# Kernel optimization log

Measured on AMD Instinct MI355X. Metric: run time of the kernel, lower is better.

The kernel has to match this reference:

```python
import jax, jax.numpy as jnp
import numpy as np
from jax.ops import segment_sum, segment_max

E = 300000
H = 256
NC = 20000
EPS = 1e-6
RESIDUAL_UNIFORM = 0.2


def setup_inputs() -> dict:
    key = jax.random.key(0)
    k = jax.random.split(key, 6)
    edge_repr = jax.random.normal(k[0], (E, H), dtype=jnp.float32)
    edge_weight = jax.random.uniform(k[1], (E,), dtype=jnp.float32)
    case_idx = jax.random.randint(k[2], (E,), 0, NC)
    W1 = jax.random.normal(k[3], (4 * H, H), dtype=jnp.float32) * (1.0 / np.sqrt(4 * H))
    b1 = jnp.zeros((H,), dtype=jnp.float32)
    W2 = jax.random.normal(k[4], (H, 1), dtype=jnp.float32) * (1.0 / np.sqrt(H))
    b2 = jnp.zeros((1,), dtype=jnp.float32)
    return {"edge_repr": edge_repr, "edge_weight": edge_weight, "case_idx": case_idx,
            "num_case": NC, "W1": W1, "b1": b1, "W2": W2, "b2": b2}


def reference(edge_repr, edge_weight, case_idx, num_case, W1, b1, W2, b2):
    # --- leave-one-out context per edge ---
    weighted = edge_repr * edge_weight[:, None]                       # [E,H]
    case_deg = segment_sum(edge_weight, case_idx, num_segments=num_case)   # [NC]
    case_sum = segment_sum(weighted, case_idx, num_segments=num_case)      # [NC,H]
    base_case_repr = case_sum / jnp.maximum(case_deg, EPS)[:, None]        # [NC,H]

    edge_case_deg = case_deg[case_idx][:, None]                       # [E,1]
    w2d = edge_weight[:, None]
    remaining = edge_case_deg - w2d
    ctx_loocv = (case_sum[case_idx] - weighted) / jnp.maximum(remaining, 1e-8)
    fallback = (remaining <= EPS).astype(edge_repr.dtype)
    ctx = fallback * base_case_repr[case_idx] + (1.0 - fallback) * ctx_loocv  # [E,H]

    # --- attention MLP on [e, ctx, e*ctx, |e-ctx|] ---
    feat = jnp.concatenate([edge_repr, ctx, edge_repr * ctx,
                            jnp.abs(edge_repr - ctx)], axis=-1)       # [E,4H]
    h = jax.nn.relu(feat @ W1 + b1)                                   # [E,H] (dropout = identity in eval)
    logits = (h @ W2 + b2)[:, 0]                                      # [E]

    # --- grouped (per-case) stable softmax ---
    gmax = segment_max(logits, case_idx, num_segments=num_case)
    gmax = jnp.where(jnp.isneginf(gmax), jnp.zeros_like(gmax), gmax)
    exp_val = jnp.exp(logits - gmax[case_idx])
    gsum = segment_sum(exp_val, case_idx, num_segments=num_case)
    alpha = exp_val / (gsum[case_idx] + 1e-8)

    uniform_alpha = edge_weight / (case_deg[case_idx] + 1e-8)
    final_alpha = (1.0 - RESIDUAL_UNIFORM) * alpha + RESIDUAL_UNIFORM * uniform_alpha

    case_repr = segment_sum(final_alpha[:, None] * edge_repr, case_idx,
                            num_segments=num_case)                    # [NC,H]
    return case_repr
```

## Files before the change

kernel.cpp:

```cpp
#include <hip/hip_runtime.h>
#include <hip/hip_bf16.h>
#include <math.h>

#define H 256
#define EPSV 1e-6f

typedef __attribute__((ext_vector_type(8))) short bf16x8;
typedef __attribute__((ext_vector_type(4))) float f32x4;
typedef __attribute__((ext_vector_type(4))) unsigned int uint4v;

static __device__ __forceinline__ unsigned short f2bf(float x){
  union { float f; unsigned u; } v; v.f = x;
  unsigned r = v.u + 0x7FFF + ((v.u >> 16) & 1);
  return (unsigned short)(r >> 16);
}
static __device__ __forceinline__ unsigned pk2(unsigned short lo, unsigned short hi){
  return (unsigned)lo | ((unsigned)hi << 16);
}

__global__ void count_kernel(const int* __restrict__ cidx, int* __restrict__ counts, int E){
  int e = blockIdx.x * blockDim.x + threadIdx.x;
  if (e < E) atomicAdd(&counts[cidx[e]], 1);
}

__global__ __launch_bounds__(1024) void scan_offsets(const int* __restrict__ counts,
                                                     int* __restrict__ offsets, int n){
  __shared__ int a[1024];
  int tid = threadIdx.x;
  int per = (n + 1023) >> 10;
  int start = tid * per;
  int end = min(start + per, n);
  int s = 0;
  for (int i = start; i < end; ++i) s += counts[i];
  a[tid] = s;
  __syncthreads();
  for (int d = 1; d < 1024; d <<= 1){
    int v = 0;
    if (tid >= d) v = a[tid - d];
    __syncthreads();
    if (tid >= d) a[tid] += v;
    __syncthreads();
  }
  int run = a[tid] - s;
  for (int i = start; i < end; ++i){ offsets[i] = run; run += counts[i]; }
  if (tid == 1023) offsets[n] = a[1023];
}

__global__ void fill_kernel(const int* __restrict__ cidx, int* __restrict__ cursor,
                            const int* __restrict__ offs, int* __restrict__ elist, int E){
  int e = blockIdx.x * blockDim.x + threadIdx.x;
  if (e < E){
    int c = cidx[e];
    int pos = atomicAdd(&cursor[c], 1);
    elist[offs[c] + pos] = e;
  }
}

__global__ __launch_bounds__(64) void sort_lists(int* __restrict__ elist,
                                                 const int* __restrict__ offs, int nc){
  int c = blockIdx.x, lane = threadIdx.x;
  int s = offs[c], e = offs[c + 1];
  int n = e - s;
  if (n <= 1) return;
  __shared__ int vals[128];
  if (n <= 128){
    int v0 = (lane < n)      ? elist[s + lane]      : 0;
    int v1 = (64 + lane < n) ? elist[s + 64 + lane] : 0;
    vals[lane] = v0; vals[64 + lane] = v1;
    __syncthreads();
    int r0 = 0, r1 = 0;
    for (int j = 0; j < n; ++j){
      int vj = vals[j];
      r0 += (vj < v0); r1 += (vj < v1);
    }
    if (lane < n)      elist[s + r0] = v0;
    if (64 + lane < n) elist[s + r1] = v1;
  } else if (lane == 0){
    for (int i = s + 1; i < e; ++i){
      int v = elist[i];
      int j = i - 1;
      while (j >= s && elist[j] > v){ elist[j + 1] = elist[j]; --j; }
      elist[j + 1] = v;
    }
  }
}

__global__ void w1_convert(const float* __restrict__ W1, unsigned short* __restrict__ w1t2){
  int t = blockIdx.x * blockDim.x + threadIdx.x;
  int k = t >> 8, n = t & 255;
  w1t2[((size_t)(k >> 5) * 256 + n) * 32 + (k & 31)] = f2bf(W1[t]);
}

__global__ __launch_bounds__(64) void case_sums(const float* __restrict__ er,
                                                const float* __restrict__ ew,
                                                const int* __restrict__ elist,
                                                const int* __restrict__ offs,
                                                float* __restrict__ csum,
                                                float* __restrict__ cdeg){
  int c = blockIdx.x, lane = threadIdx.x;
  int s = offs[c], e = offs[c + 1];
  f32x4 acc = (f32x4){0.f,0.f,0.f,0.f};
  float dacc = 0.f;
  int i = s;
  for (; i + 1 < e; i += 2){
    int e1 = elist[i], e2 = elist[i + 1];
    float w1 = ew[e1], w2 = ew[e2];
    f32x4 v1 = *(const f32x4*)&er[(size_t)e1 * H + lane * 4];
    f32x4 v2 = *(const f32x4*)&er[(size_t)e2 * H + lane * 4];
    acc += v1 * w1;
    acc += v2 * w2;
    dacc += w1; dacc += w2;
  }
  if (i < e){
    int e1 = elist[i];
    float w1 = ew[e1];
    acc += (*(const f32x4*)&er[(size_t)e1 * H + lane * 4]) * w1;
    dacc += w1;
  }
  *(f32x4*)&csum[(size_t)c * H + lane * 4] = acc;
  if (lane == 0) cdeg[c] = dacc;
}

__global__ __launch_bounds__(256, 2) void fused_mlp(
    const float* __restrict__ er, const float* __restrict__ ew,
    const int* __restrict__ cidx, const float* __restrict__ cdeg,
    const float* __restrict__ csum, const unsigned short* __restrict__ w1t2,
    const float* __restrict__ b1, const float* __restrict__ w2,
    const float* __restrict__ b2, float* __restrict__ logits, int E)
{
  __shared__ unsigned short fl[4][64 * 64];
  __shared__ float lpart[4][64];
  int tid = threadIdx.x;
  long e0 = (long)blockIdx.x * 64;

  int wn = tid >> 6, lane = tid & 63;
  int l15 = lane & 15, lg = lane >> 4;

  int r = tid >> 2, q = tid & 3;
  long e = e0 + r;
  bool valid = (e < (long)E);
  int   cce = valid ? cidx[e] : 0;
  float w   = valid ? ew[e]   : 0.f;
  float deg = valid ? cdeg[cce] : 1.f;
  float rem = deg - w;
  bool  fb  = (rem <= EPSV);
  float inv  = fb ? (1.0f / fmaxf(deg, EPSV)) : (1.0f / fmaxf(rem, 1e-8f));
  float wsel = fb ? 0.f : w;
  const float* erow = er   + (size_t)e   * H + q * 16;
  const float* srow = csum + (size_t)cce * H + q * 16;
  unsigned rowb = (unsigned)r * 64u;
  unsigned swz  = ((unsigned)(r & 7)) << 3;

  f32x4 acc[4][4];
  #pragma unroll
  for (int mt = 0; mt < 4; ++mt)
    #pragma unroll
    for (int nt = 0; nt < 4; ++nt) acc[mt][nt] = (f32x4){0.f,0.f,0.f,0.f};

  unsigned bpcol = ((unsigned)(wn * 64 + l15)) * 32u + (unsigned)lg * 8u;

  f32x4 xr[4] = {(f32x4){0,0,0,0},(f32x4){0,0,0,0},(f32x4){0,0,0,0},(f32x4){0,0,0,0}};
  f32x4 sr[4] = {(f32x4){0,0,0,0},(f32x4){0,0,0,0},(f32x4){0,0,0,0},(f32x4){0,0,0,0}};

#define LOADQ(QT)                                                         \
  if (valid){                                                             \
    _Pragma("unroll")                                                     \
    for (int j = 0; j < 4; ++j){                                          \
      xr[j] = *(const f32x4*)(erow + (QT) * 64 + 4 * j);                  \
      sr[j] = *(const f32x4*)(srow + (QT) * 64 + 4 * j);                  \
    }                                                                     \
  }

#define CLUSTER(CL)                                                       \
  {                                                                       \
    const int kg_ = ((CL) & 3) * 8 + qt * 2 + ((CL) >> 2);                \
    bf16x8 bfr[4];                                                        \
    _Pragma("unroll")                                                     \
    for (int nt = 0; nt < 4; ++nt)                                        \
      bfr[nt] = *(const bf16x8*)(w1t2 + (size_t)kg_ * 8192 + nt * 512 + bpcol); \
    const int sg_ = (CL) & 3;                                             \
    unsigned eb_ = (unsigned)(((CL) >> 2) * 32 + lg * 8);                 \
    _Pragma("unroll")                                                     \
    for (int mt = 0; mt < 4; ++mt){                                       \
      unsigned row_ = (unsigned)(mt * 16 + l15);                          \
      unsigned off_ = row_ * 64u + (eb_ ^ ((row_ & 7u) << 3));            \
      bf16x8 af_ = *(const bf16x8*)&fl[sg_][off_];                        \
      _Pragma("unroll")                                                   \
      for (int nt = 0; nt < 4; ++nt)                                      \
        acc[mt][nt] = __builtin_amdgcn_mfma_f32_16x16x32_bf16(af_, bfr[nt], acc[mt][nt], 0, 0, 0); \
    }                                                                     \
  }

  LOADQ(0)

  #pragma unroll
  for (int qt = 0; qt < 4; ++qt){
    #pragma unroll
    for (int j2 = 0; j2 < 2; ++j2){
      unsigned xw[4], cw[4], pw[4], dw[4];
      #pragma unroll
      for (int d = 0; d < 4; ++d){
        float x0 = xr[2*j2 + (d>>1)][(d&1)*2+0], x1 = xr[2*j2 + (d>>1)][(d&1)*2+1];
        float s0 = sr[2*j2 + (d>>1)][(d&1)*2+0], s1 = sr[2*j2 + (d>>1)][(d&1)*2+1];
        float c0 = (s0 - wsel * x0) * inv;
        float c1 = (s1 - wsel * x1) * inv;
        xw[d] = pk2(f2bf(x0), f2bf(x1));
        cw[d] = pk2(f2bf(c0), f2bf(c1));
        pw[d] = pk2(f2bf(x0 * c0), f2bf(x1 * c1));
        dw[d] = pk2(f2bf(fabsf(x0 - c0)), f2bf(fabsf(x1 - c1)));
      }
      unsigned elem = (unsigned)(q * 16 + j2 * 8);
      unsigned off  = rowb + (elem ^ swz);
      *(uint4v*)&fl[0][off] = (uint4v){xw[0], xw[1], xw[2], xw[3]};
      *(uint4v*)&fl[1][off] = (uint4v){cw[0], cw[1], cw[2], cw[3]};
      *(uint4v*)&fl[2][off] = (uint4v){pw[0], pw[1], pw[2], pw[3]};
      *(uint4v*)&fl[3][off] = (uint4v){dw[0], dw[1], dw[2], dw[3]};
    }
    __syncthreads();
    if (qt == 0){ LOADQ(1) } else if (qt == 1){ LOADQ(2) } else if (qt == 2){ LOADQ(3) }

    CLUSTER(0) CLUSTER(1) CLUSTER(2) CLUSTER(3)
    CLUSTER(4) CLUSTER(5) CLUSTER(6) CLUSTER(7)
    __syncthreads();
  }
#undef LOADQ
#undef CLUSTER

  float p[4][4];
  #pragma unroll
  for (int mt = 0; mt < 4; ++mt)
    #pragma unroll
    for (int j = 0; j < 4; ++j) p[mt][j] = 0.f;

  #pragma unroll
  for (int nt = 0; nt < 4; ++nt){
    int col = wn * 64 + nt * 16 + l15;
    float b1c = b1[col], w2c = w2[col];
    #pragma unroll
    for (int mt = 0; mt < 4; ++mt)
      #pragma unroll
      for (int j = 0; j < 4; ++j)
        p[mt][j] += fmaxf(acc[mt][nt][j] + b1c, 0.f) * w2c;
  }
  #pragma unroll
  for (int mask = 1; mask < 16; mask <<= 1)
    #pragma unroll
    for (int mt = 0; mt < 4; ++mt)
      #pragma unroll
      for (int j = 0; j < 4; ++j)
        p[mt][j] += __shfl_xor(p[mt][j], mask);

  if (l15 == 0){
    #pragma unroll
    for (int mt = 0; mt < 4; ++mt)
      #pragma unroll
      for (int j = 0; j < 4; ++j)
        lpart[wn][mt * 16 + lg * 4 + j] = p[mt][j];
  }
  __syncthreads();
  if (tid < 64 && e0 + tid < (long)E)
    logits[e0 + tid] = lpart[0][tid] + lpart[1][tid] + lpart[2][tid] + lpart[3][tid] + b2[0];
}

__global__ __launch_bounds__(64) void finalize(
    const float* __restrict__ er, const float* __restrict__ ew,
    const float* __restrict__ logits, const int* __restrict__ elist,
    const int* __restrict__ offs, const float* __restrict__ cdeg,
    float* __restrict__ out)
{
  int c = blockIdx.x, lane = threadIdx.x;
  int s = offs[c], e = offs[c + 1];
  int n = e - s;
  if (n == 0){
    *(f32x4*)&out[(size_t)c * H + lane * 4] = (f32x4){0.f,0.f,0.f,0.f};
    return;
  }

  float m = -INFINITY;
  for (int i = lane; i < n; i += 64) m = fmaxf(m, logits[elist[s + i]]);
  #pragma unroll
  for (int mask = 32; mask > 0; mask >>= 1) m = fmaxf(m, __shfl_xor(m, mask));

  float sm = 0.f;
  for (int i = lane; i < n; i += 64) sm += expf(logits[elist[s + i]] - m);
  #pragma unroll
  for (int mask = 32; mask > 0; mask >>= 1) sm += __shfl_xor(sm, mask);

  float gsum = sm + 1e-8f;
  float degc = cdeg[c] + 1e-8f;

  __shared__ float fa[256];
  f32x4 acc = (f32x4){0.f,0.f,0.f,0.f};
  for (int base = 0; base < n; base += 256){
    int chunk = min(n - base, 256);
    for (int i = lane; i < chunk; i += 64){
      int ed = elist[s + base + i];
      fa[i] = 0.8f * expf(logits[ed] - m) / gsum + 0.2f * ew[ed] / degc;
    }
    __syncthreads();
    int i = 0;
    for (; i + 1 < chunk; i += 2){
      int ed0 = elist[s + base + i], ed1 = elist[s + base + i + 1];
      f32x4 v0 = *(const f32x4*)&er[(size_t)ed0 * H + lane * 4];
      f32x4 v1 = *(const f32x4*)&er[(size_t)ed1 * H + lane * 4];
      acc += fa[i] * v0;
      acc += fa[i + 1] * v1;
    }
    if (i < chunk){
      int ed0 = elist[s + base + i];
      acc += fa[i] * (*(const f32x4*)&er[(size_t)ed0 * H + lane * 4]);
    }
    __syncthreads();
  }
  *(f32x4*)&out[(size_t)c * H + lane * 4] = acc;
}

extern "C" void kernel_launch(void* const* d_in, const int* in_sizes, int n_in,
                              void* d_out, int out_size, void* d_ws, size_t ws_size,
                              hipStream_t stream){
  const float* er  = (const float*)d_in[0];
  const float* ew  = (const float*)d_in[1];
  const int*   cid = (const int*)d_in[2];
  const float* W1  = (const float*)d_in[4];
  const float* b1  = (const float*)d_in[5];
  const float* W2  = (const float*)d_in[6];
  const float* b2  = (const float*)d_in[7];
  float* out = (float*)d_out;

  int E  = in_sizes[1];
  int NC = out_size / H;

  char* ws = (char*)d_ws;
  auto al = [](size_t x){ return (x + 255) & ~(size_t)255; };
  size_t o = 0;
  int* counts = (int*)(ws + o);  o = al(o + (size_t)NC * 4);
  int* cursor = (int*)(ws + o);  o = al(o + (size_t)NC * 4);
  int* offs   = (int*)(ws + o);  o = al(o + (size_t)(NC + 1) * 4);
  int* elist  = (int*)(ws + o);  o = al(o + (size_t)E * 4);
  float* cdeg = (float*)(ws + o); o = al(o + (size_t)NC * 4);
  float* csum = (float*)(ws + o); o = al(o + (size_t)NC * H * 4);
  float* logits = (float*)(ws + o); o = al(o + (size_t)E * 4);
  unsigned short* w1t2 = (unsigned short*)(ws + o); o = al(o + (size_t)1024 * H * 2);

  hipMemsetAsync(counts, 0, (size_t)NC * 4, stream);
  hipMemsetAsync(cursor, 0, (size_t)NC * 4, stream);

  count_kernel<<<(E + 255) / 256, 256, 0, stream>>>(cid, counts, E);
  scan_offsets<<<1, 1024, 0, stream>>>(counts, offs, NC);
  fill_kernel<<<(E + 255) / 256, 256, 0, stream>>>(cid, cursor, offs, elist, E);
  sort_lists<<<NC, 64, 0, stream>>>(elist, offs, NC);
  w1_convert<<<(1024 * H) / 256, 256, 0, stream>>>(W1, w1t2);
  case_sums<<<NC, 64, 0, stream>>>(er, ew, elist, offs, csum, cdeg);
  fused_mlp<<<(E + 63) / 64, 256, 0, stream>>>(er, ew, cid, cdeg, csum, w1t2, b1, W2, b2, logits, E);
  finalize<<<NC, 64, 0, stream>>>(er, ew, logits, elist, offs, cdeg, out);
}
```

Measured before the change: 448.1 us.

## Stage W1 tiles into LDS via async global_load_lds with double buffering

The fused MLP kernel stops reading W1 fragments from global memory straight into registers. It now stages bf16 W1 chunks into a double-buffered LDS region using global_load_lds, and the W1 conversion writes a pre-swizzled layout that matches the LDS layout. The K loop is restructured into 8 steps of 32 features per segment, with manual waitcnt placement so the next B stage and the next activation load overlap the MFMA clusters. The cost is more LDS per block (which may reduce occupancy), hand-tuned waitcnt counts that are fragile to get right, and invalid rows now handled by masking loads instead of skipping them.

```diff
diff --git a/kernel.cpp b/kernel.cpp
--- a/kernel.cpp
+++ b/kernel.cpp
@@ -85,10 +85,14 @@
   }
 }
 
-__global__ void w1_convert(const float* __restrict__ W1, unsigned short* __restrict__ w1t2){
+__global__ void w1_convert(const float* __restrict__ W1, unsigned short* __restrict__ w1t2s){
   int t = blockIdx.x * blockDim.x + threadIdx.x;
   int k = t >> 8, n = t & 255;
-  w1t2[((size_t)(k >> 5) * 256 + n) * 32 + (k & 31)] = f2bf(W1[t]);
+  int kg = k >> 5, klo = k & 31;
+  unsigned b = (unsigned)((n & 63) * 64 + klo * 2);
+  b ^= ((b >> 7) & 3u) << 4;
+  size_t byteaddr = (size_t)kg * 16384 + (size_t)(n >> 6) * 4096 + b;
+  w1t2s[byteaddr >> 1] = f2bf(W1[t]);
 }
 
 __global__ __launch_bounds__(64) void case_sums(const float* __restrict__ er,
@@ -124,11 +128,12 @@
 __global__ __launch_bounds__(256, 2) void fused_mlp(
     const float* __restrict__ er, const float* __restrict__ ew,
     const int* __restrict__ cidx, const float* __restrict__ cdeg,
-    const float* __restrict__ csum, const unsigned short* __restrict__ w1t2,
+    const float* __restrict__ csum, const unsigned short* __restrict__ w1t2s,
     const float* __restrict__ b1, const float* __restrict__ w2,
     const float* __restrict__ b2, float* __restrict__ logits, int E)
 {
-  __shared__ unsigned short fl[4][64 * 64];
+  __shared__ __align__(16) unsigned short featl[4 * 2048];
+  __shared__ __align__(16) unsigned short Bst[2 * 8192];
   __shared__ float lpart[4][64];
   int tid = threadIdx.x;
   long e0 = (long)blockIdx.x * 64;
@@ -139,17 +144,18 @@
   int r = tid >> 2, q = tid & 3;
   long e = e0 + r;
   bool valid = (e < (long)E);
-  int   cce = valid ? cidx[e] : 0;
-  float w   = valid ? ew[e]   : 0.f;
+  long ec = valid ? e : 0;
+  int   cce = cidx[ec];
+  float w   = valid ? ew[ec] : 0.f;
   float deg = valid ? cdeg[cce] : 1.f;
   float rem = deg - w;
   bool  fb  = (rem <= EPSV);
   float inv  = fb ? (1.0f / fmaxf(deg, EPSV)) : (1.0f / fmaxf(rem, 1e-8f));
   float wsel = fb ? 0.f : w;
-  const float* erow = er   + (size_t)e   * H + q * 16;
-  const float* srow = csum + (size_t)cce * H + q * 16;
-  unsigned rowb = (unsigned)r * 64u;
-  unsigned swz  = ((unsigned)(r & 7)) << 3;
+  float vm   = valid ? 1.f : 0.f;
+  const float* erow = er   + (size_t)ec  * H + q * 8;
+  const float* srow = csum + (size_t)cce * H + q * 8;
+  unsigned packoff = (unsigned)r * 32u + ((unsigned)(q ^ ((r >> 1) & 3))) * 8u;
 
   f32x4 acc[4][4];
   #pragma unroll
@@ -157,51 +163,56 @@
     #pragma unroll
     for (int nt = 0; nt < 4; ++nt) acc[mt][nt] = (f32x4){0.f,0.f,0.f,0.f};
 
-  unsigned bpcol = ((unsigned)(wn * 64 + l15)) * 32u + (unsigned)lg * 8u;
-
-  f32x4 xr[4] = {(f32x4){0,0,0,0},(f32x4){0,0,0,0},(f32x4){0,0,0,0},(f32x4){0,0,0,0}};
-  f32x4 sr[4] = {(f32x4){0,0,0,0},(f32x4){0,0,0,0},(f32x4){0,0,0,0},(f32x4){0,0,0,0}};
-
-#define LOADQ(QT)                                                         \
-  if (valid){                                                             \
-    _Pragma("unroll")                                                     \
-    for (int j = 0; j < 4; ++j){                                          \
-      xr[j] = *(const f32x4*)(erow + (QT) * 64 + 4 * j);                  \
-      sr[j] = *(const f32x4*)(srow + (QT) * 64 + 4 * j);                  \
-    }                                                                     \
-  }
-
-#define CLUSTER(CL)                                                       \
-  {                                                                       \
-    const int kg_ = ((CL) & 3) * 8 + qt * 2 + ((CL) >> 2);                \
-    bf16x8 bfr[4];                                                        \
-    _Pragma("unroll")                                                     \
-    for (int nt = 0; nt < 4; ++nt)                                        \
-      bfr[nt] = *(const bf16x8*)(w1t2 + (size_t)kg_ * 8192 + nt * 512 + bpcol); \
-    const int sg_ = (CL) & 3;                                             \
-    unsigned eb_ = (unsigned)(((CL) >> 2) * 32 + lg * 8);                 \
-    _Pragma("unroll")                                                     \
-    for (int mt = 0; mt < 4; ++mt){                                       \
-      unsigned row_ = (unsigned)(mt * 16 + l15);                          \
-      unsigned off_ = row_ * 64u + (eb_ ^ ((row_ & 7u) << 3));            \
-      bf16x8 af_ = *(const bf16x8*)&fl[sg_][off_];                        \
-      _Pragma("unroll")                                                   \
-      for (int nt = 0; nt < 4; ++nt)                                      \
-        acc[mt][nt] = __builtin_amdgcn_mfma_f32_16x16x32_bf16(af_, bfr[nt], acc[mt][nt], 0, 0, 0); \
-    }                                                                     \
-  }
-
+  f32x4 xr[2], sr[2];
+
+#define LOADQ(HH)                                                          \
+  { xr[0] = *(const f32x4*)(erow + (HH) * 32);                             \
+    xr[1] = *(const f32x4*)(erow + (HH) * 32 + 4);                         \
+    sr[0] = *(const f32x4*)(srow + (HH) * 32);                             \
+    sr[1] = *(const f32x4*)(srow + (HH) * 32 + 4); }
+
+#define STAGE(BUF, KG)                                                     \
+  { const char* gb_ = (const char*)w1t2s + ((size_t)(KG) * 16384 +         \
+                      (size_t)wn * 4096 + (size_t)lane * 16);              \
+    char* lb_ = (char*)Bst + ((BUF) * 16384 + wn * 4096 + lane * 16);      \
+    __builtin_amdgcn_global_load_lds((const __attribute__((address_space(1))) void*)gb_,            (__attribute__((address_space(3))) void*)lb_,            16, 0, 0); \
+    __builtin_amdgcn_global_load_lds((const __attribute__((address_space(1))) void*)(gb_ + 1024),   (__attribute__((address_space(3))) void*)(lb_ + 1024),   16, 0, 0); \
+    __builtin_amdgcn_global_load_lds((const __attribute__((address_space(1))) void*)(gb_ + 2048),   (__attribute__((address_space(3))) void*)(lb_ + 2048),   16, 0, 0); \
+    __builtin_amdgcn_global_load_lds((const __attribute__((address_space(1))) void*)(gb_ + 3072),   (__attribute__((address_space(3))) void*)(lb_ + 3072),   16, 0, 0); }
+
+#define CLUSTER(SG, BUF)                                                   \
+  { bf16x8 bfr[4];                                                         \
+    _Pragma("unroll")                                                      \
+    for (int nt = 0; nt < 4; ++nt){                                        \
+      unsigned lcol_ = (unsigned)(nt * 16 + l15);                          \
+      unsigned by_ = (BUF) * 16384u + (unsigned)wn * 4096u + lcol_ * 64u   \
+                   + (((unsigned)lg ^ ((lcol_ >> 1) & 3u)) * 16u);         \
+      bfr[nt] = *(const bf16x8*)((const char*)Bst + by_);                  \
+    }                                                                      \
+    _Pragma("unroll")                                                      \
+    for (int mt = 0; mt < 4; ++mt){                                        \
+      unsigned rr_ = (unsigned)(mt * 16 + l15);                            \
+      unsigned le_ = ((unsigned)lg ^ ((rr_ >> 1) & 3u)) * 8u;              \
+      bf16x8 afr = *(const bf16x8*)&featl[(SG) * 2048u + rr_ * 32u + le_]; \
+      _Pragma("unroll")                                                    \
+      for (int nt = 0; nt < 4; ++nt)                                       \
+        acc[mt][nt] = __builtin_amdgcn_mfma_f32_16x16x32_bf16(afr, bfr[nt], acc[mt][nt], 0, 0, 0); \
+    }                                                                      \
+  }
+
+  STAGE(0, 0)
+  STAGE(1, 8)
   LOADQ(0)
 
-  #pragma unroll
-  for (int qt = 0; qt < 4; ++qt){
-    #pragma unroll
-    for (int j2 = 0; j2 < 2; ++j2){
+  #pragma unroll 1
+  for (int h = 0; h < 8; ++h){
+    int hn = (h + 1) & 7;
+    {
       unsigned xw[4], cw[4], pw[4], dw[4];
       #pragma unroll
       for (int d = 0; d < 4; ++d){
-        float x0 = xr[2*j2 + (d>>1)][(d&1)*2+0], x1 = xr[2*j2 + (d>>1)][(d&1)*2+1];
-        float s0 = sr[2*j2 + (d>>1)][(d&1)*2+0], s1 = sr[2*j2 + (d>>1)][(d&1)*2+1];
+        float x0 = xr[d >> 1][(d & 1) * 2 + 0] * vm, x1 = xr[d >> 1][(d & 1) * 2 + 1] * vm;
+        float s0 = sr[d >> 1][(d & 1) * 2 + 0] * vm, s1 = sr[d >> 1][(d & 1) * 2 + 1] * vm;
         float c0 = (s0 - wsel * x0) * inv;
         float c1 = (s1 - wsel * x1) * inv;
         xw[d] = pk2(f2bf(x0), f2bf(x1));
@@ -209,21 +220,33 @@
         pw[d] = pk2(f2bf(x0 * c0), f2bf(x1 * c1));
         dw[d] = pk2(f2bf(fabsf(x0 - c0)), f2bf(fabsf(x1 - c1)));
       }
-      unsigned elem = (unsigned)(q * 16 + j2 * 8);
-      unsigned off  = rowb + (elem ^ swz);
-      *(uint4v*)&fl[0][off] = (uint4v){xw[0], xw[1], xw[2], xw[3]};
-      *(uint4v*)&fl[1][off] = (uint4v){cw[0], cw[1], cw[2], cw[3]};
-      *(uint4v*)&fl[2][off] = (uint4v){pw[0], pw[1], pw[2], pw[3]};
-      *(uint4v*)&fl[3][off] = (uint4v){dw[0], dw[1], dw[2], dw[3]};
-    }
-    __syncthreads();
-    if (qt == 0){ LOADQ(1) } else if (qt == 1){ LOADQ(2) } else if (qt == 2){ LOADQ(3) }
-
-    CLUSTER(0) CLUSTER(1) CLUSTER(2) CLUSTER(3)
-    CLUSTER(4) CLUSTER(5) CLUSTER(6) CLUSTER(7)
-    __syncthreads();
-  }
+      *(uint4v*)&featl[0 * 2048 + packoff] = (uint4v){xw[0], xw[1], xw[2], xw[3]};
+      *(uint4v*)&featl[1 * 2048 + packoff] = (uint4v){cw[0], cw[1], cw[2], cw[3]};
+      *(uint4v*)&featl[2 * 2048 + packoff] = (uint4v){pw[0], pw[1], pw[2], pw[3]};
+      *(uint4v*)&featl[3 * 2048 + packoff] = (uint4v){dw[0], dw[1], dw[2], dw[3]};
+    }
+    __syncthreads();
+
+    CLUSTER(0, 0)
+    asm volatile("s_waitcnt lgkmcnt(0)" ::: "memory");
+    STAGE(0, 16 + h)
+    CLUSTER(1, 1)
+    asm volatile("s_waitcnt lgkmcnt(0)" ::: "memory");
+    STAGE(1, 24 + h)
+    LOADQ(hn)
+    asm volatile("s_waitcnt vmcnt(8)" ::: "memory");
+    CLUSTER(2, 0)
+    asm volatile("s_waitcnt lgkmcnt(0)" ::: "memory");
+    STAGE(0, hn)
+    asm volatile("s_waitcnt vmcnt(8)" ::: "memory");
+    CLUSTER(3, 1)
+    asm volatile("s_waitcnt lgkmcnt(0)" ::: "memory");
+    STAGE(1, 8 + hn)
+    __syncthreads();
+  }
+  asm volatile("" :: "v"(xr[0][0]), "v"(xr[1][0]), "v"(sr[0][0]), "v"(sr[1][0]));
 #undef LOADQ
+#undef STAGE
 #undef CLUSTER
 
   float p[4][4];
@@ -340,7 +363,7 @@
   float* cdeg = (float*)(ws + o); o = al(o + (size_t)NC * 4);
   float* csum = (float*)(ws + o); o = al(o + (size_t)NC * H * 4);
   float* logits = (float*)(ws + o); o = al(o + (size_t)E * 4);
-  unsigned short* w1t2 = (unsigned short*)(ws + o); o = al(o + (size_t)1024 * H * 2);
+  unsigned short* w1t2s = (unsigned short*)(ws + o); o = al(o + (size_t)1024 * H * 2);
 
   hipMemsetAsync(counts, 0, (size_t)NC * 4, stream);
   hipMemsetAsync(cursor, 0, (size_t)NC * 4, stream);
@@ -349,8 +372,8 @@
   scan_offsets<<<1, 1024, 0, stream>>>(counts, offs, NC);
   fill_kernel<<<(E + 255) / 256, 256, 0, stream>>>(cid, cursor, offs, elist, E);
   sort_lists<<<NC, 64, 0, stream>>>(elist, offs, NC);
-  w1_convert<<<(1024 * H) / 256, 256, 0, stream>>>(W1, w1t2);
+  w1_convert<<<(1024 * H) / 256, 256, 0, stream>>>(W1, w1t2s);
   case_sums<<<NC, 64, 0, stream>>>(er, ew, elist, offs, csum, cdeg);
-  fused_mlp<<<(E + 63) / 64, 256, 0, stream>>>(er, ew, cid, cdeg, csum, w1t2, b1, W2, b2, logits, E);
+  fused_mlp<<<(E + 63) / 64, 256, 0, stream>>>(er, ew, cid, cdeg, csum, w1t2s, b1, W2, b2, logits, E);
   finalize<<<NC, 64, 0, stream>>>(er, ew, logits, elist, offs, cdeg, out);
 }
```

After: 405.2 us. 9.6% less time.
